# Kernel optimization log

Hardware: AMD Instinct MI355X
Metric: run time of the kernel (lower is better)

Reference implementation:

```python
import jax, jax.numpy as jnp
import numpy as np

ALPHA = 0.2      # LeakyReLU negative slope
NEG_INF = -9e15  # mask value from original code

def setup_inputs() -> dict:
    key = jax.random.key(0)
    k1, k2, k3, k4 = jax.random.split(key, 4)
    N, R, Fin, Fout = 4096, 4, 256, 64
    return {
        "h": jax.random.normal(k1, (N, Fin), dtype=jnp.float32),
        "edge_attr": jax.random.normal(k2, (R, N, N), dtype=jnp.float32),
        "W": jax.random.normal(k3, (Fin, Fout), dtype=jnp.float32) * 0.05,
        "a": jax.random.normal(k4, (2 * Fout, 1), dtype=jnp.float32) * 0.05,
    }

def reference(h, edge_attr, W, a):
    Fout = W.shape[1]
    R, N, _ = edge_attr.shape
    Wh = h @ W                                   # [N, Fout]
    Wh1 = Wh @ a[:Fout]                          # [N, 1]
    Wh2 = Wh @ a[Fout:]                          # [N, 1]
    e = jax.nn.leaky_relu(Wh1 + Wh2.T, ALPHA)    # [N, N]
    e = e[None, :, :] * edge_attr                # [R, N, N]
    e = jnp.where(edge_attr > 0, e, NEG_INF)
    e = jax.nn.softmax(e, axis=1)                # softmax over dim=1 (faithful)
    # dropout p=0.0 / eval mode -> identity
    h_prime = jnp.einsum('rij,jf->rif', e, Wh)   # [R, N, Fout]
    # torch.cat along dim=1 of R tensors of [N, Fout] -> [N, R*Fout]
    h_cat = jnp.transpose(h_prime, (1, 0, 2)).reshape(N, R * Fout)
    return jax.nn.elu(h_cat), e
```

## Files before the change

### kernel.cpp

```cpp
#include <hip/hip_runtime.h>
#include <hip/hip_bf16.h>
#include <math.h>

#define PN    4096
#define PR    4
#define PFIN  256
#define PFOUT 64
#define PALPHA 0.2f
#define INVN  (1.0f/4096.0f)

__global__ __launch_bounds__(256) void p1_kernel(
    const float* __restrict__ h, const float* __restrict__ W,
    const float* __restrict__ a,
    float* __restrict__ wh, float* __restrict__ wh1, float* __restrict__ wh2)
{
    const int t  = threadIdx.x;
    const int f  = t & 63;
    const int rg = t >> 6;
    const int i0 = blockIdx.x * 16 + rg * 4;
    const float* h0 = h + (size_t)i0 * PFIN;
    const float av1 = a[f];
    const float av2 = a[64 + f];
    float a0 = 0.f, a1 = 0.f, a2 = 0.f, a3 = 0.f;
#pragma unroll 4
    for (int k = 0; k < PFIN; ++k) {
        const float wv = W[k * PFOUT + f];
        a0 = fmaf(h0[k],            wv, a0);
        a1 = fmaf(h0[PFIN + k],     wv, a1);
        a2 = fmaf(h0[2 * PFIN + k], wv, a2);
        a3 = fmaf(h0[3 * PFIN + k], wv, a3);
    }
    float* o = wh + (size_t)i0 * PFOUT + f;
    o[0]         = a0;
    o[PFOUT]     = a1;
    o[2 * PFOUT] = a2;
    o[3 * PFOUT] = a3;

    float s0 = a0 * av1, s1 = a1 * av1, s2 = a2 * av1, s3 = a3 * av1;
    float u0 = a0 * av2, u1 = a1 * av2, u2 = a2 * av2, u3 = a3 * av2;
#pragma unroll
    for (int m = 1; m < 64; m <<= 1) {
        s0 += __shfl_xor(s0, m, 64);
        s1 += __shfl_xor(s1, m, 64);
        s2 += __shfl_xor(s2, m, 64);
        s3 += __shfl_xor(s3, m, 64);
        u0 += __shfl_xor(u0, m, 64);
        u1 += __shfl_xor(u1, m, 64);
        u2 += __shfl_xor(u2, m, 64);
        u3 += __shfl_xor(u3, m, 64);
    }
    if (f == 0) {
        wh1[i0]     = s0; wh1[i0 + 1] = s1; wh1[i0 + 2] = s2; wh1[i0 + 3] = s3;
        wh2[i0]     = u0; wh2[i0 + 1] = u1; wh2[i0 + 2] = u2; wh2[i0 + 3] = u3;
    }
}

__global__ __launch_bounds__(256) void p2_kernel(
    const float* __restrict__ edge_r, const float* __restrict__ wh1,
    const float* __restrict__ wh2, float* __restrict__ csum_r,
    float* __restrict__ eout_r)
{
    const int t  = threadIdx.x;
    const int jt = blockIdx.x;
    const int is = blockIdx.y;
    const int j  = jt * 1024 + t * 4;
    const int ib = is * 32;
    const float4 w2 = *(const float4*)(wh2 + j);
    const float4* e4 = (const float4*)(edge_r + (size_t)ib * PN + jt * 1024);
    float4*       o4 = (float4*)(eout_r + (size_t)ib * PN + jt * 1024);
    float s0 = 0.f, s1 = 0.f, s2 = 0.f, s3 = 0.f;
#pragma unroll 4
    for (int ii = 0; ii < 32; ++ii) {
        const float w1  = wh1[ib + ii];
        const float4 ev = e4[(size_t)ii * (PN / 4) + t];
        float b0 = w1 + w2.x; b0 = fmaxf(b0, PALPHA * b0);
        float b1 = w1 + w2.y; b1 = fmaxf(b1, PALPHA * b1);
        float b2 = w1 + w2.z; b2 = fmaxf(b2, PALPHA * b2);
        float b3 = w1 + w2.w; b3 = fmaxf(b3, PALPHA * b3);
        const float x0 = (ev.x > 0.f) ? __expf(b0 * ev.x) : 0.f;
        const float x1 = (ev.y > 0.f) ? __expf(b1 * ev.y) : 0.f;
        const float x2 = (ev.z > 0.f) ? __expf(b2 * ev.z) : 0.f;
        const float x3 = (ev.w > 0.f) ? __expf(b3 * ev.w) : 0.f;
        o4[(size_t)ii * (PN / 4) + t] = make_float4(x0, x1, x2, x3);
        s0 += x0; s1 += x1; s2 += x2; s3 += x3;
    }
    atomicAdd(csum_r + j,     s0);
    atomicAdd(csum_r + j + 1, s1);
    atomicAdd(csum_r + j + 2, s2);
    atomicAdd(csum_r + j + 3, s3);
}

__global__ __launch_bounds__(256) void p3_kernel(
    float* __restrict__ eout_r, const float* __restrict__ wh,
    const float* __restrict__ csum_r, float* __restrict__ part)
{
    __shared__ float4 ET[64 * 32];
    __shared__ float4 WL[64 * 16];

    const int t  = threadIdx.x;
    const int it = blockIdx.x;
    const int js = blockIdx.y;
    const int i0 = it * 128;
    const int jc = t & 63;
    const int ih = t >> 6;
    const int tf = t & 7;
    const int tr = t >> 3;

    float acc[4][8];
#pragma unroll
    for (int p = 0; p < 4; ++p)
#pragma unroll
        for (int q = 0; q < 8; ++q) acc[p][q] = 0.f;

    const float4* whg4 = (const float4*)wh;

    for (int c = 0; c < 4; ++c) {
        const int j0 = js * 256 + c * 64;
        const int jg = j0 + jc;
        const float cs   = csum_r[jg];
        const float cinv = (cs > 0.f) ? 1.0f / cs : 0.f;

        __syncthreads();

#pragma unroll
        for (int u = 0; u < 4; ++u) {
            const int idx = t + u * 256;
            WL[idx] = whg4[(size_t)j0 * 16 + idx];
        }

#pragma unroll
        for (int k = 0; k < 8; ++k) {
            const int q  = ih * 8 + k;
            const int il = q * 4;
            float* ep = eout_r + (size_t)(i0 + il) * PN + jg;
            const float e0 = ep[0];
            const float e1 = ep[PN];
            const float e2 = ep[2 * PN];
            const float e3 = ep[3 * PN];
            const float en0 = (cs > 0.f) ? e0 * cinv : INVN;
            const float en1 = (cs > 0.f) ? e1 * cinv : INVN;
            const float en2 = (cs > 0.f) ? e2 * cinv : INVN;
            const float en3 = (cs > 0.f) ? e3 * cinv : INVN;
            ep[0]      = en0;
            ep[PN]     = en1;
            ep[2 * PN] = en2;
            ep[3 * PN] = en3;
            ET[(jc << 5) | (q ^ (jc & 31))] = make_float4(en0, en1, en2, en3);
        }
        __syncthreads();

#pragma unroll 2
        for (int jj = 0; jj < 64; ++jj) {
            const float4 ea = ET[(jj << 5) | (tr ^ (jj & 31))];
            const float4 wa = WL[(jj << 4) | (tf * 2)];
            const float4 wb = WL[(jj << 4) | (tf * 2 + 1)];
            const float ev_[4] = {ea.x, ea.y, ea.z, ea.w};
            const float wv_[8] = {wa.x, wa.y, wa.z, wa.w, wb.x, wb.y, wb.z, wb.w};
#pragma unroll
            for (int p = 0; p < 4; ++p)
#pragma unroll
                for (int q = 0; q < 8; ++q)
                    acc[p][q] = fmaf(ev_[p], wv_[q], acc[p][q]);
        }
    }

#pragma unroll
    for (int p = 0; p < 4; ++p) {
        float* pp = part + ((size_t)js * PN + (i0 + tr * 4 + p)) * PFOUT + tf * 8;
        *(float4*)pp       = make_float4(acc[p][0], acc[p][1], acc[p][2], acc[p][3]);
        *(float4*)(pp + 4) = make_float4(acc[p][4], acc[p][5], acc[p][6], acc[p][7]);
    }
}

__global__ __launch_bounds__(256) void p4_kernel(
    const float* __restrict__ part, float* __restrict__ out1_r)
{
    const int idx = blockIdx.x * 256 + threadIdx.x;
    const int i   = idx >> 4;
    const int fq  = idx & 15;
    const float4* pp = (const float4*)part;
    float sx = 0.f, sy = 0.f, sz = 0.f, sw = 0.f;
#pragma unroll
    for (int sj = 0; sj < 16; ++sj) {
        const float4 v = pp[((size_t)sj * PN + i) * 16 + fq];
        sx += v.x; sy += v.y; sz += v.z; sw += v.w;
    }
    float4 o;
    o.x = (sx > 0.f) ? sx : expm1f(sx);
    o.y = (sy > 0.f) ? sy : expm1f(sy);
    o.z = (sz > 0.f) ? sz : expm1f(sz);
    o.w = (sw > 0.f) ? sw : expm1f(sw);
    *(float4*)(out1_r + (size_t)i * (PR * PFOUT) + fq * 4) = o;
}

extern "C" void kernel_launch(void* const* d_in, const int* in_sizes, int n_in,
                              void* d_out, int out_size, void* d_ws, size_t ws_size,
                              hipStream_t stream)
{
    const float* h    = (const float*)d_in[0];
    const float* edge = (const float*)d_in[1];
    const float* W    = (const float*)d_in[2];
    const float* a    = (const float*)d_in[3];

    float* out1 = (float*)d_out;
    float* eout = (float*)d_out + (size_t)PN * PR * PFOUT;

    float* ws   = (float*)d_ws;
    float* wh   = ws;
    float* wh1  = ws + 262144;
    float* wh2  = ws + 266240;
    float* csum = ws + 270336;
    float* part = ws + 286720;

    hipMemsetAsync(csum, 0, (size_t)PR * PN * sizeof(float), stream);
    p1_kernel<<<256, 256, 0, stream>>>(h, W, a, wh, wh1, wh2);

    for (int r = 0; r < PR; ++r) {
        float* er_out = eout + (size_t)r * PN * PN;
        p2_kernel<<<dim3(4, 128), 256, 0, stream>>>(
            edge + (size_t)r * PN * PN, wh1, wh2, csum + r * PN, er_out);
        p3_kernel<<<dim3(32, 16), 256, 0, stream>>>(
            er_out, wh, csum + r * PN, part);
        p4_kernel<<<256, 256, 0, stream>>>(part, out1 + r * PFOUT);
    }
}
```

Baseline: 708.4 us.

## Recompute attention exponentials in the matmul pass instead of storing and rereading

The column-sum pass now only reads edge_attr and writes per-slab partial sums, reduced by a separate kernel, which removes the atomics, the memset and the full unnormalized write of the attention matrix. The matmul kernel rereads edge_attr, recomputes the exponentials, normalizes them, writes the final attention once and uses larger 256x512 tiles with 8x8 register blocking. All relations are batched into single launches along a z grid dimension, and p1 stages h through shared memory. This trades one read-modify-write pass over the large attention output for a second read of edge_attr plus recomputed exps, and adds register pressure in p3.

```diff
diff --git a/kernel.cpp b/kernel.cpp
--- a/kernel.cpp
+++ b/kernel.cpp
@@ -14,13 +14,22 @@
     const float* __restrict__ a,
     float* __restrict__ wh, float* __restrict__ wh1, float* __restrict__ wh2)
 {
+    __shared__ float hL[16 * PFIN];
     const int t  = threadIdx.x;
     const int f  = t & 63;
     const int rg = t >> 6;
-    const int i0 = blockIdx.x * 16 + rg * 4;
-    const float* h0 = h + (size_t)i0 * PFIN;
+    const int i0 = blockIdx.x * 16;
+    const int ir = i0 + rg * 4;
+
+    const float4* hg4 = (const float4*)(h + (size_t)i0 * PFIN);
+    float4* hL4 = (float4*)hL;
+#pragma unroll
+    for (int u = 0; u < 4; ++u) hL4[t + 256 * u] = hg4[t + 256 * u];
+    __syncthreads();
+
     const float av1 = a[f];
     const float av2 = a[64 + f];
+    const float* h0 = hL + (rg * 4) * PFIN;
     float a0 = 0.f, a1 = 0.f, a2 = 0.f, a3 = 0.f;
 #pragma unroll 4
     for (int k = 0; k < PFIN; ++k) {
@@ -30,7 +39,7 @@
         a2 = fmaf(h0[2 * PFIN + k], wv, a2);
         a3 = fmaf(h0[3 * PFIN + k], wv, a3);
     }
-    float* o = wh + (size_t)i0 * PFOUT + f;
+    float* o = wh + (size_t)ir * PFOUT + f;
     o[0]         = a0;
     o[PFOUT]     = a1;
     o[2 * PFOUT] = a2;
@@ -50,139 +59,174 @@
         u3 += __shfl_xor(u3, m, 64);
     }
     if (f == 0) {
-        wh1[i0]     = s0; wh1[i0 + 1] = s1; wh1[i0 + 2] = s2; wh1[i0 + 3] = s3;
-        wh2[i0]     = u0; wh2[i0 + 1] = u1; wh2[i0 + 2] = u2; wh2[i0 + 3] = u3;
-    }
-}
-
-__global__ __launch_bounds__(256) void p2_kernel(
-    const float* __restrict__ edge_r, const float* __restrict__ wh1,
-    const float* __restrict__ wh2, float* __restrict__ csum_r,
-    float* __restrict__ eout_r)
+        wh1[ir]     = s0; wh1[ir + 1] = s1; wh1[ir + 2] = s2; wh1[ir + 3] = s3;
+        wh2[ir]     = u0; wh2[ir + 1] = u1; wh2[ir + 2] = u2; wh2[ir + 3] = u3;
+    }
+}
+
+__global__ __launch_bounds__(256) void p2s_kernel(
+    const float* __restrict__ edge, const float* __restrict__ wh1,
+    const float* __restrict__ wh2, float* __restrict__ pcs)
 {
     const int t  = threadIdx.x;
     const int jt = blockIdx.x;
     const int is = blockIdx.y;
+    const int r  = blockIdx.z;
     const int j  = jt * 1024 + t * 4;
-    const int ib = is * 32;
+    const int ib = is * 64;
     const float4 w2 = *(const float4*)(wh2 + j);
-    const float4* e4 = (const float4*)(edge_r + (size_t)ib * PN + jt * 1024);
-    float4*       o4 = (float4*)(eout_r + (size_t)ib * PN + jt * 1024);
+    const float4* e4 = (const float4*)(edge + ((size_t)r * PN + ib) * PN + jt * 1024);
     float s0 = 0.f, s1 = 0.f, s2 = 0.f, s3 = 0.f;
 #pragma unroll 4
-    for (int ii = 0; ii < 32; ++ii) {
+    for (int ii = 0; ii < 64; ++ii) {
         const float w1  = wh1[ib + ii];
         const float4 ev = e4[(size_t)ii * (PN / 4) + t];
         float b0 = w1 + w2.x; b0 = fmaxf(b0, PALPHA * b0);
         float b1 = w1 + w2.y; b1 = fmaxf(b1, PALPHA * b1);
         float b2 = w1 + w2.z; b2 = fmaxf(b2, PALPHA * b2);
         float b3 = w1 + w2.w; b3 = fmaxf(b3, PALPHA * b3);
-        const float x0 = (ev.x > 0.f) ? __expf(b0 * ev.x) : 0.f;
-        const float x1 = (ev.y > 0.f) ? __expf(b1 * ev.y) : 0.f;
-        const float x2 = (ev.z > 0.f) ? __expf(b2 * ev.z) : 0.f;
-        const float x3 = (ev.w > 0.f) ? __expf(b3 * ev.w) : 0.f;
-        o4[(size_t)ii * (PN / 4) + t] = make_float4(x0, x1, x2, x3);
-        s0 += x0; s1 += x1; s2 += x2; s3 += x3;
-    }
-    atomicAdd(csum_r + j,     s0);
-    atomicAdd(csum_r + j + 1, s1);
-    atomicAdd(csum_r + j + 2, s2);
-    atomicAdd(csum_r + j + 3, s3);
+        s0 += (ev.x > 0.f) ? __expf(b0 * ev.x) : 0.f;
+        s1 += (ev.y > 0.f) ? __expf(b1 * ev.y) : 0.f;
+        s2 += (ev.z > 0.f) ? __expf(b2 * ev.z) : 0.f;
+        s3 += (ev.w > 0.f) ? __expf(b3 * ev.w) : 0.f;
+    }
+    *(float4*)(pcs + ((size_t)r * 64 + is) * PN + j) = make_float4(s0, s1, s2, s3);
+}
+
+__global__ __launch_bounds__(256) void p2b_kernel(
+    const float* __restrict__ pcs, float* __restrict__ csum)
+{
+    const int idx = blockIdx.x * 256 + threadIdx.x;
+    const int r   = idx >> 12;
+    const int j   = idx & 4095;
+    float s = 0.f;
+#pragma unroll
+    for (int is = 0; is < 64; ++is)
+        s += pcs[((size_t)r * 64 + is) * PN + j];
+    csum[idx] = s;
 }
 
 __global__ __launch_bounds__(256) void p3_kernel(
-    float* __restrict__ eout_r, const float* __restrict__ wh,
-    const float* __restrict__ csum_r, float* __restrict__ part)
-{
-    __shared__ float4 ET[64 * 32];
+    const float* __restrict__ edge, const float* __restrict__ wh,
+    const float* __restrict__ wh1, const float* __restrict__ wh2,
+    const float* __restrict__ csum, float* __restrict__ eout,
+    float* __restrict__ part)
+{
+    __shared__ float4 ET[256 * 16];
     __shared__ float4 WL[64 * 16];
 
     const int t  = threadIdx.x;
     const int it = blockIdx.x;
     const int js = blockIdx.y;
-    const int i0 = it * 128;
-    const int jc = t & 63;
-    const int ih = t >> 6;
+    const int r  = blockIdx.z;
+    const int i0 = it * 256;
+    const int cq = t & 15;
+    const int rg = t >> 4;
     const int tf = t & 7;
     const int tr = t >> 3;
 
-    float acc[4][8];
-#pragma unroll
-    for (int p = 0; p < 4; ++p)
+    float acc[8][8];
+#pragma unroll
+    for (int p = 0; p < 8; ++p)
 #pragma unroll
         for (int q = 0; q < 8; ++q) acc[p][q] = 0.f;
 
-    const float4* whg4 = (const float4*)wh;
-
-    for (int c = 0; c < 4; ++c) {
-        const int j0 = js * 256 + c * 64;
-        const int jg = j0 + jc;
-        const float cs   = csum_r[jg];
-        const float cinv = (cs > 0.f) ? 1.0f / cs : 0.f;
+    const float* edge_r = edge + (size_t)r * PN * PN;
+    float*       eout_r = eout + (size_t)r * PN * PN;
+    const float* csum_r = csum + r * PN;
+    const float4* whg4  = (const float4*)wh;
+
+    for (int c = 0; c < 8; ++c) {
+        const int j0 = js * 512 + c * 64;
+        const int jq = j0 + cq * 4;
+        const float4 cs4 = *(const float4*)(csum_r + jq);
+        const float4 w2  = *(const float4*)(wh2 + jq);
+        const float i0x = (cs4.x > 0.f) ? 1.0f / cs4.x : 0.f;
+        const float i1x = (cs4.y > 0.f) ? 1.0f / cs4.y : 0.f;
+        const float i2x = (cs4.z > 0.f) ? 1.0f / cs4.z : 0.f;
+        const float i3x = (cs4.w > 0.f) ? 1.0f / cs4.w : 0.f;
+        const float m0 = (cs4.x > 0.f) ? 0.f : INVN;
+        const float m1 = (cs4.y > 0.f) ? 0.f : INVN;
+        const float m2 = (cs4.z > 0.f) ? 0.f : INVN;
+        const float m3 = (cs4.w > 0.f) ? 0.f : INVN;
 
         __syncthreads();
 
 #pragma unroll
-        for (int u = 0; u < 4; ++u) {
-            const int idx = t + u * 256;
-            WL[idx] = whg4[(size_t)j0 * 16 + idx];
-        }
-
-#pragma unroll
-        for (int k = 0; k < 8; ++k) {
-            const int q  = ih * 8 + k;
-            const int il = q * 4;
-            float* ep = eout_r + (size_t)(i0 + il) * PN + jg;
-            const float e0 = ep[0];
-            const float e1 = ep[PN];
-            const float e2 = ep[2 * PN];
-            const float e3 = ep[3 * PN];
-            const float en0 = (cs > 0.f) ? e0 * cinv : INVN;
-            const float en1 = (cs > 0.f) ? e1 * cinv : INVN;
-            const float en2 = (cs > 0.f) ? e2 * cinv : INVN;
-            const float en3 = (cs > 0.f) ? e3 * cinv : INVN;
-            ep[0]      = en0;
-            ep[PN]     = en1;
-            ep[2 * PN] = en2;
-            ep[3 * PN] = en3;
-            ET[(jc << 5) | (q ^ (jc & 31))] = make_float4(en0, en1, en2, en3);
+        for (int u = 0; u < 4; ++u)
+            WL[t + 256 * u] = whg4[(size_t)j0 * 16 + t + 256 * u];
+
+#pragma unroll 4
+        for (int k = 0; k < 16; ++k) {
+            const int row = rg + k * 16;
+            const int gi  = i0 + row;
+            const float4 ev = *(const float4*)(edge_r + (size_t)gi * PN + jq);
+            const float  w1 = wh1[gi];
+            float b0 = w1 + w2.x; b0 = fmaxf(b0, PALPHA * b0);
+            float b1 = w1 + w2.y; b1 = fmaxf(b1, PALPHA * b1);
+            float b2 = w1 + w2.z; b2 = fmaxf(b2, PALPHA * b2);
+            float b3 = w1 + w2.w; b3 = fmaxf(b3, PALPHA * b3);
+            float4 en;
+            en.x = (ev.x > 0.f) ? __expf(b0 * ev.x) * i0x : m0;
+            en.y = (ev.y > 0.f) ? __expf(b1 * ev.y) * i1x : m1;
+            en.z = (ev.z > 0.f) ? __expf(b2 * ev.z) * i2x : m2;
+            en.w = (ev.w > 0.f) ? __expf(b3 * ev.w) * i3x : m3;
+            *(float4*)(eout_r + (size_t)gi * PN + jq) = en;
+            ET[(row << 4) | (cq ^ ((row >> 3) & 7))] = en;
         }
         __syncthreads();
 
-#pragma unroll 2
-        for (int jj = 0; jj < 64; ++jj) {
-            const float4 ea = ET[(jj << 5) | (tr ^ (jj & 31))];
-            const float4 wa = WL[(jj << 4) | (tf * 2)];
-            const float4 wb = WL[(jj << 4) | (tf * 2 + 1)];
-            const float ev_[4] = {ea.x, ea.y, ea.z, ea.w};
-            const float wv_[8] = {wa.x, wa.y, wa.z, wa.w, wb.x, wb.y, wb.z, wb.w};
-#pragma unroll
-            for (int p = 0; p < 4; ++p)
-#pragma unroll
-                for (int q = 0; q < 8; ++q)
-                    acc[p][q] = fmaf(ev_[p], wv_[q], acc[p][q]);
+        for (int jjq = 0; jjq < 16; ++jjq) {
+            float4 ev[8];
+#pragma unroll
+            for (int p = 0; p < 8; ++p) {
+                const int row = tr * 8 + p;
+                ev[p] = ET[(row << 4) | (jjq ^ (tr & 7))];
+            }
+#pragma unroll
+            for (int u = 0; u < 4; ++u) {
+                const int jj = jjq * 4 + u;
+                const float4 wa = WL[(jj << 4) | (tf * 2)];
+                const float4 wb = WL[(jj << 4) | (tf * 2 + 1)];
+#pragma unroll
+                for (int p = 0; p < 8; ++p) {
+                    const float epv = (u == 0) ? ev[p].x :
+                                      (u == 1) ? ev[p].y :
+                                      (u == 2) ? ev[p].z : ev[p].w;
+                    acc[p][0] = fmaf(epv, wa.x, acc[p][0]);
+                    acc[p][1] = fmaf(epv, wa.y, acc[p][1]);
+                    acc[p][2] = fmaf(epv, wa.z, acc[p][2]);
+                    acc[p][3] = fmaf(epv, wa.w, acc[p][3]);
+                    acc[p][4] = fmaf(epv, wb.x, acc[p][4]);
+                    acc[p][5] = fmaf(epv, wb.y, acc[p][5]);
+                    acc[p][6] = fmaf(epv, wb.z, acc[p][6]);
+                    acc[p][7] = fmaf(epv, wb.w, acc[p][7]);
+                }
+            }
         }
     }
 
 #pragma unroll
-    for (int p = 0; p < 4; ++p) {
-        float* pp = part + ((size_t)js * PN + (i0 + tr * 4 + p)) * PFOUT + tf * 8;
+    for (int p = 0; p < 8; ++p) {
+        float* pp = part + (((size_t)js * PR + r) * PN + (i0 + tr * 8 + p)) * PFOUT + tf * 8;
         *(float4*)pp       = make_float4(acc[p][0], acc[p][1], acc[p][2], acc[p][3]);
         *(float4*)(pp + 4) = make_float4(acc[p][4], acc[p][5], acc[p][6], acc[p][7]);
     }
 }
 
 __global__ __launch_bounds__(256) void p4_kernel(
-    const float* __restrict__ part, float* __restrict__ out1_r)
-{
-    const int idx = blockIdx.x * 256 + threadIdx.x;
-    const int i   = idx >> 4;
-    const int fq  = idx & 15;
+    const float* __restrict__ part, float* __restrict__ out1)
+{
+    const int o4 = blockIdx.x * 256 + threadIdx.x;
+    const int i  = o4 >> 6;
+    const int c4 = o4 & 63;
+    const int r  = c4 >> 4;
+    const int fq = c4 & 15;
     const float4* pp = (const float4*)part;
     float sx = 0.f, sy = 0.f, sz = 0.f, sw = 0.f;
 #pragma unroll
-    for (int sj = 0; sj < 16; ++sj) {
-        const float4 v = pp[((size_t)sj * PN + i) * 16 + fq];
+    for (int sj = 0; sj < 8; ++sj) {
+        const float4 v = pp[(((size_t)sj * PR + r) * PN + i) * 16 + fq];
         sx += v.x; sy += v.y; sz += v.z; sw += v.w;
     }
     float4 o;
@@ -190,7 +234,7 @@
     o.y = (sy > 0.f) ? sy : expm1f(sy);
     o.z = (sz > 0.f) ? sz : expm1f(sz);
     o.w = (sw > 0.f) ? sw : expm1f(sw);
-    *(float4*)(out1_r + (size_t)i * (PR * PFOUT) + fq * 4) = o;
+    ((float4*)out1)[o4] = o;
 }
 
 extern "C" void kernel_launch(void* const* d_in, const int* in_sizes, int n_in,
@@ -210,17 +254,12 @@
     float* wh1  = ws + 262144;
     float* wh2  = ws + 266240;
     float* csum = ws + 270336;
-    float* part = ws + 286720;
-
-    hipMemsetAsync(csum, 0, (size_t)PR * PN * sizeof(float), stream);
-    p1_kernel<<<256, 256, 0, stream>>>(h, W, a, wh, wh1, wh2);
-
-    for (int r = 0; r < PR; ++r) {
-        float* er_out = eout + (size_t)r * PN * PN;
-        p2_kernel<<<dim3(4, 128), 256, 0, stream>>>(
-            edge + (size_t)r * PN * PN, wh1, wh2, csum + r * PN, er_out);
-        p3_kernel<<<dim3(32, 16), 256, 0, stream>>>(
-            er_out, wh, csum + r * PN, part);
-        p4_kernel<<<256, 256, 0, stream>>>(part, out1 + r * PFOUT);
-    }
-}
+    float* pcs  = ws + 286720;
+    float* part = ws + 1335296;
+
+    p1_kernel <<<256, 256, 0, stream>>>(h, W, a, wh, wh1, wh2);
+    p2s_kernel<<<dim3(4, 64, 4), 256, 0, stream>>>(edge, wh1, wh2, pcs);
+    p2b_kernel<<<64, 256, 0, stream>>>(pcs, csum);
+    p3_kernel <<<dim3(16, 8, 4), 256, 0, stream>>>(edge, wh, wh1, wh2, csum, eout, part);
+    p4_kernel <<<1024, 256, 0, stream>>>(part, out1);
+}
```

Result: faster. 606.3 us (-14.4%).
